# Performance work log

Hardware: AMD Instinct MI355X
Metric: run time of the kernel (lower is better)

The kernel has to match this reference:

```python
import jax, jax.numpy as jnp
import numpy as np

NUM_PRIMARY_CAPS = 8
PRIMARY_DIM = 8
NUM_CLASSES = 10
OUT_DIM = 16
CHANNELS = 32
NUM_ROUTING = 3
IN_UNITS1 = CHANNELS * 20 * 20  # 12800


def squash(s):
    # squash as written in the source: |s| / (1 + |s|^2) * s
    n = jnp.linalg.norm(s, axis=-1, keepdims=True)
    return n / (1.0 + n * n) * s


def routing(u_hat, num_routing):
    # u_hat: [B, num_caps, in_units, dim_caps]
    b = jnp.zeros(u_hat.shape[:3] + (1,), dtype=u_hat.dtype)
    v = None
    for it in range(num_routing):
        c = jax.nn.softmax(b, axis=1)                       # over num_caps
        s = jnp.sum(c * u_hat, axis=2, keepdims=True)        # [B,J,1,M]
        v = squash(s)
        if it < num_routing - 1:
            b = b + jnp.sum(u_hat * v, axis=-1, keepdims=True)
    return v[:, :, 0, :]                                     # [B, num_caps, dim_caps]


def setup_inputs() -> dict:
    key = jax.random.key(0)
    k1, k2, k3, k4, k5 = jax.random.split(key, 5)
    x = jax.random.normal(k1, (64, 1, 28, 28), dtype=jnp.float32)
    conv_w = jax.random.normal(k2, (CHANNELS, 1, 9, 9), dtype=jnp.float32) * 0.05
    conv_b = jax.random.normal(k3, (CHANNELS,), dtype=jnp.float32) * 0.05
    # W: [num_capsules, in_units, dim_capsules, in_channels]
    W1 = jax.random.normal(k4, (NUM_PRIMARY_CAPS, IN_UNITS1, PRIMARY_DIM, CHANNELS), dtype=jnp.float32) * 0.05
    W2 = jax.random.normal(k5, (NUM_CLASSES, NUM_PRIMARY_CAPS, OUT_DIM, PRIMARY_DIM), dtype=jnp.float32) * 0.05
    return {"x": x, "conv_w": conv_w, "conv_b": conv_b, "W1": W1, "W2": W2}


def reference(x, conv_w, conv_b, W1, W2):
    B = x.shape[0]
    # conv1 + relu: [B,1,28,28] -> [B,C,20,20]
    h = jax.lax.conv_general_dilated(
        x, conv_w, window_strides=(1, 1), padding='VALID',
        dimension_numbers=('NCHW', 'OIHW', 'NCHW'))
    h = jax.nn.relu(h + conv_b[None, :, None, None])
    # primary capsules: flatten features to in_units; the source einsum
    # 'ijkl,ijkm->ijkm' reduces W over its in_channels axis and broadcasts x,
    # so u_hat[b,j,k,m] = sum_c W1[j,k,m,c] * x[b,k]
    xf = h.reshape(B, IN_UNITS1)
    u1 = jnp.einsum('jkmc,bk->bjkm', W1, xf)   # [B, 8, 12800, primary_dim]
    v1 = routing(u1, 1)                         # [B, 8, primary_dim]
    # digit capsules: per-unit feature vectors, standard capsule transform
    u2 = jnp.einsum('jkmc,bkc->bjkm', W2, v1)   # [B, 10, 8, out_dim]
    v2 = routing(u2, NUM_ROUTING)               # [B, 10, out_dim]
    return v2
```

## Files before the change

kernel.cpp:

```cpp
#include <hip/hip_runtime.h>

typedef float f4 __attribute__((ext_vector_type(4)));

__device__ __forceinline__ float readlane_f(float v, int l) {
    return __int_as_float(__builtin_amdgcn_readlane(__float_as_int(v), l));
}

__device__ __forceinline__ void barrier_lds() {
    asm volatile("s_waitcnt lgkmcnt(0)\n\ts_barrier" ::: "memory");
}

__global__ __launch_bounds__(512) void fused_kernel(
    const float* __restrict__ X, const float* __restrict__ CW, const float* __restrict__ CB,
    const float* __restrict__ W1, float* __restrict__ S1P)
{
    int i = blockIdx.x;
    int c = i >> 3, p0 = (i & 7) * 50;
    int t = threadIdx.x;
    int wave = t >> 6, lane = t & 63;

    __shared__ float xs[64][309];
    __shared__ float xt[50][64];

    int py0 = p0 / 20;

    int k0 = c * 400 + p0;
    const f4* Wp = reinterpret_cast<const f4*>(W1) + (size_t)wave * 819200
                   + (size_t)k0 * 64 + lane;
    f4 pre[10];
    #pragma unroll
    for (int q = 0; q < 10; ++q)
        pre[q] = __builtin_nontemporal_load(Wp + (size_t)q * 64);

    float bias = CB[c];
    const float* wcg = CW + c * 81;
    float w[81];
    #pragma unroll
    for (int q = 0; q < 81; ++q) w[q] = wcg[q];

    {
        int b = t >> 3, q = t & 7;
        const f4* src = reinterpret_cast<const f4*>(X + (size_t)b * 784 + py0 * 28);
        #pragma unroll
        for (int s = 0; s < 10; ++s) {
            int idx4 = q + 8 * s;
            if (idx4 < 77) {
                f4 v = src[idx4];
                float* d = &xs[b][idx4 * 4];
                d[0] = v.x; d[1] = v.y; d[2] = v.z; d[3] = v.w;
            }
        }
    }
    barrier_lds();

    {
        int psub = wave, b = lane;
        for (int pl = psub; pl < 50; pl += 8) {
            int p = p0 + pl;
            int py = p / 20, px = p - py * 20;
            const float* xrow = &xs[b][(py - py0) * 28 + px];
            float acc = bias;
            #pragma unroll
            for (int dy = 0; dy < 9; ++dy)
                #pragma unroll
                for (int dx = 0; dx < 9; ++dx)
                    acc = fmaf(xrow[dy * 28 + dx], w[dy * 9 + dx], acc);
            xt[pl][b] = acc > 0.f ? acc : 0.f;
        }
    }
    barrier_lds();

    float acc[8] = {0.f,0.f,0.f,0.f,0.f,0.f,0.f,0.f};
    #pragma unroll
    for (int kk = 0; kk < 10; ++kk) {
        f4 wv = pre[kk];
        float xv = xt[kk][lane];
        float s = (wv.x + wv.y) + (wv.z + wv.w);
        s += __shfl_xor(s, 1);
        s += __shfl_xor(s, 2);
        s += __shfl_xor(s, 4);
        #pragma unroll
        for (int m = 0; m < 8; ++m)
            acc[m] = fmaf(xv, readlane_f(s, m * 8), acc[m]);
    }
    Wp += (size_t)10 * 64;
    #pragma unroll 10
    for (int kk = 10; kk < 50; ++kk) {
        f4 wv = __builtin_nontemporal_load(Wp); Wp += 64;
        float xv = xt[kk][lane];
        float s = (wv.x + wv.y) + (wv.z + wv.w);
        s += __shfl_xor(s, 1);
        s += __shfl_xor(s, 2);
        s += __shfl_xor(s, 4);
        #pragma unroll
        for (int m = 0; m < 8; ++m)
            acc[m] = fmaf(xv, readlane_f(s, m * 8), acc[m]);
    }

    float* dst = S1P + (((size_t)i * 64 + lane) * 8 + wave) * 8;
    f4 lo = {acc[0], acc[1], acc[2], acc[3]};
    f4 hi = {acc[4], acc[5], acc[6], acc[7]};
    reinterpret_cast<f4*>(dst)[0] = lo;
    reinterpret_cast<f4*>(dst)[1] = hi;
}

__global__ __launch_bounds__(256) void routing_kernel(
    const float* __restrict__ W2, const float* __restrict__ S1P,
    float* __restrict__ OUT)
{
    int b = blockIdx.x;
    int t = threadIdx.x;
    __shared__ float part[16][64];
    __shared__ float v1[64];
    __shared__ float u2[10][8][16];
    __shared__ float blog[10][8];
    __shared__ float cw[10][8];
    __shared__ float sv[10][16];
    __shared__ float vv[10][16];
    __shared__ float fac[16];

    {
        int q = t & 15, r = t >> 4;
        const f4* base = reinterpret_cast<const f4*>(S1P) + ((size_t)r * 64 + b) * 16 + q;
        f4 a = {0.f, 0.f, 0.f, 0.f};
        #pragma unroll
        for (int s = 0; s < 16; ++s)
            a += base[(size_t)s * 16384];
        part[r][q * 4 + 0] = a.x;
        part[r][q * 4 + 1] = a.y;
        part[r][q * 4 + 2] = a.z;
        part[r][q * 4 + 3] = a.w;
    }
    __syncthreads();
    if (t < 64) {
        float v = 0.f;
        #pragma unroll
        for (int r = 0; r < 16; ++r) v += part[r][t];
        v1[t] = v * 0.125f;
    }
    if (t >= 64 && t < 144) { int q = t - 64; blog[q >> 3][q & 7] = 0.f; }
    __syncthreads();
    if (t < 8) {
        float n2 = 0.f;
        #pragma unroll
        for (int m = 0; m < 8; ++m) { float x = v1[t * 8 + m]; n2 = fmaf(x, x, n2); }
        float n = sqrtf(n2);
        fac[t] = n / (1.f + n2);
    }
    __syncthreads();
    if (t < 64) v1[t] *= fac[t >> 3];
    __syncthreads();

    for (int idx = t; idx < 1280; idx += 256) {
        int j = idx >> 7;
        int r = idx & 127;
        int k = r >> 4, m = r & 15;
        const float* wp = W2 + idx * 8;
        float a = 0.f;
        #pragma unroll
        for (int cc = 0; cc < 8; ++cc) a = fmaf(wp[cc], v1[k * 8 + cc], a);
        u2[j][k][m] = a;
    }
    __syncthreads();

    for (int it = 0; it < 3; ++it) {
        if (t < 8) {
            float mx = -1e30f;
            #pragma unroll
            for (int j = 0; j < 10; ++j) mx = fmaxf(mx, blog[j][t]);
            float e[10], se = 0.f;
            #pragma unroll
            for (int j = 0; j < 10; ++j) { e[j] = expf(blog[j][t] - mx); se += e[j]; }
            float inv = 1.f / se;
            #pragma unroll
            for (int j = 0; j < 10; ++j) cw[j][t] = e[j] * inv;
        }
        __syncthreads();
        if (t < 160) {
            int j = t >> 4, m = t & 15;
            float a = 0.f;
            #pragma unroll
            for (int k = 0; k < 8; ++k) a = fmaf(cw[j][k], u2[j][k][m], a);
            sv[j][m] = a;
        }
        __syncthreads();
        if (t < 10) {
            float n2 = 0.f;
            #pragma unroll
            for (int m = 0; m < 16; ++m) { float x = sv[t][m]; n2 = fmaf(x, x, n2); }
            float n = sqrtf(n2);
            fac[t] = n / (1.f + n2);
        }
        __syncthreads();
        if (t < 160) { int j = t >> 4, m = t & 15; vv[j][m] = sv[j][m] * fac[j]; }
        __syncthreads();
        if (it < 2) {
            if (t < 80) {
                int j = t >> 3, k = t & 7;
                float d = 0.f;
                #pragma unroll
                for (int m = 0; m < 16; ++m) d = fmaf(u2[j][k][m], vv[j][m], d);
                blog[j][k] += d;
            }
            __syncthreads();
        }
    }
    if (t < 160) OUT[b * 160 + t] = vv[t >> 4][t & 15];
}

extern "C" void kernel_launch(void* const* d_in, const int* in_sizes, int n_in,
                              void* d_out, int out_size, void* d_ws, size_t ws_size,
                              hipStream_t stream) {
    const float* X  = (const float*)d_in[0];
    const float* CW = (const float*)d_in[1];
    const float* CB = (const float*)d_in[2];
    const float* W1 = (const float*)d_in[3];
    const float* W2 = (const float*)d_in[4];
    float* S1P = (float*)d_ws;
    float* OUT = (float*)d_out;

    fused_kernel<<<256, 512, 0, stream>>>(X, CW, CB, W1, S1P);
    routing_kernel<<<64, 256, 0, stream>>>(W2, S1P, OUT);
}
```

Baseline: 165.5 us.

## Fuse conv/primary-capsule and routing kernels via atomic grid-wide flag barrier

Merges the two launches into one kernel. Every block writes its partial sums and then increments a global counter. The first 64 blocks spin until all 256 blocks have arrived, then run the routing stage in the same launch. To make room for the routing shared memory, the conv input staging is halved to 32 batches and processed in two passes, and the partial-sum reduction is respread over 512 threads. This aims to remove the second launch and the gap between kernels, but it adds a memset launch and relies on all 256 blocks being co-resident to avoid deadlock.

```diff
diff --git a/kernel.cpp b/kernel.cpp
--- a/kernel.cpp
+++ b/kernel.cpp
@@ -10,17 +10,26 @@
     asm volatile("s_waitcnt lgkmcnt(0)\n\ts_barrier" ::: "memory");
 }
 
-__global__ __launch_bounds__(512) void fused_kernel(
+__global__ __launch_bounds__(512) void mega_kernel(
     const float* __restrict__ X, const float* __restrict__ CW, const float* __restrict__ CB,
-    const float* __restrict__ W1, float* __restrict__ S1P)
+    const float* __restrict__ W1, const float* __restrict__ W2,
+    float* __restrict__ S1P, unsigned int* __restrict__ FLAG, float* __restrict__ OUT)
 {
     int i = blockIdx.x;
     int c = i >> 3, p0 = (i & 7) * 50;
     int t = threadIdx.x;
     int wave = t >> 6, lane = t & 63;
 
-    __shared__ float xs[64][309];
+    __shared__ float xs[32][309];
     __shared__ float xt[50][64];
+    __shared__ float part[32][64];
+    __shared__ float v1[64];
+    __shared__ float u2[10][8][16];
+    __shared__ float blog[10][8];
+    __shared__ float cw[10][8];
+    __shared__ float sv[10][16];
+    __shared__ float vv[10][16];
+    __shared__ float fac[16];
 
     int py0 = p0 / 20;
 
@@ -38,37 +47,38 @@
     #pragma unroll
     for (int q = 0; q < 81; ++q) w[q] = wcg[q];
 
-    {
-        int b = t >> 3, q = t & 7;
-        const f4* src = reinterpret_cast<const f4*>(X + (size_t)b * 784 + py0 * 28);
-        #pragma unroll
-        for (int s = 0; s < 10; ++s) {
-            int idx4 = q + 8 * s;
-            if (idx4 < 77) {
-                f4 v = src[idx4];
-                float* d = &xs[b][idx4 * 4];
-                d[0] = v.x; d[1] = v.y; d[2] = v.z; d[3] = v.w;
+    for (int h = 0; h < 2; ++h) {
+        {
+            int b2 = t >> 4, q = t & 15;
+            const f4* src = reinterpret_cast<const f4*>(X + (size_t)(b2 + 32 * h) * 784 + py0 * 28);
+            #pragma unroll
+            for (int s = 0; s < 5; ++s) {
+                int idx4 = q + 16 * s;
+                if (idx4 < 77) {
+                    f4 v = src[idx4];
+                    float* d = &xs[b2][idx4 * 4];
+                    d[0] = v.x; d[1] = v.y; d[2] = v.z; d[3] = v.w;
+                }
             }
         }
-    }
-    barrier_lds();
-
-    {
-        int psub = wave, b = lane;
-        for (int pl = psub; pl < 50; pl += 8) {
-            int p = p0 + pl;
-            int py = p / 20, px = p - py * 20;
-            const float* xrow = &xs[b][(py - py0) * 28 + px];
-            float acc = bias;
-            #pragma unroll
-            for (int dy = 0; dy < 9; ++dy)
+        barrier_lds();
+        {
+            int psub = t >> 5, b2 = t & 31;
+            for (int pl = psub; pl < 50; pl += 16) {
+                int p = p0 + pl;
+                int py = p / 20, px = p - py * 20;
+                const float* xrow = &xs[b2][(py - py0) * 28 + px];
+                float acc = bias;
                 #pragma unroll
-                for (int dx = 0; dx < 9; ++dx)
-                    acc = fmaf(xrow[dy * 28 + dx], w[dy * 9 + dx], acc);
-            xt[pl][b] = acc > 0.f ? acc : 0.f;
-        }
-    }
-    barrier_lds();
+                for (int dy = 0; dy < 9; ++dy)
+                    #pragma unroll
+                    for (int dx = 0; dx < 9; ++dx)
+                        acc = fmaf(xrow[dy * 28 + dx], w[dy * 9 + dx], acc);
+                xt[pl][b2 + 32 * h] = acc > 0.f ? acc : 0.f;
+            }
+        }
+        barrier_lds();
+    }
 
     float acc[8] = {0.f,0.f,0.f,0.f,0.f,0.f,0.f,0.f};
     #pragma unroll
@@ -97,35 +107,36 @@
             acc[m] = fmaf(xv, readlane_f(s, m * 8), acc[m]);
     }
 
-    float* dst = S1P + (((size_t)i * 64 + lane) * 8 + wave) * 8;
-    f4 lo = {acc[0], acc[1], acc[2], acc[3]};
-    f4 hi = {acc[4], acc[5], acc[6], acc[7]};
-    reinterpret_cast<f4*>(dst)[0] = lo;
-    reinterpret_cast<f4*>(dst)[1] = hi;
-}
-
-__global__ __launch_bounds__(256) void routing_kernel(
-    const float* __restrict__ W2, const float* __restrict__ S1P,
-    float* __restrict__ OUT)
-{
-    int b = blockIdx.x;
-    int t = threadIdx.x;
-    __shared__ float part[16][64];
-    __shared__ float v1[64];
-    __shared__ float u2[10][8][16];
-    __shared__ float blog[10][8];
-    __shared__ float cw[10][8];
-    __shared__ float sv[10][16];
-    __shared__ float vv[10][16];
-    __shared__ float fac[16];
+    {
+        float* dst = S1P + (((size_t)i * 64 + lane) * 8 + wave) * 8;
+        f4 lo = {acc[0], acc[1], acc[2], acc[3]};
+        f4 hi = {acc[4], acc[5], acc[6], acc[7]};
+        reinterpret_cast<f4*>(dst)[0] = lo;
+        reinterpret_cast<f4*>(dst)[1] = hi;
+    }
+
+    __syncthreads();
+    if (t == 0) {
+        __threadfence();
+        atomicAdd(FLAG, 1u);
+    }
+    if (i >= 64) return;
+
+    int b = i;
+    if (t == 0) {
+        while (__hip_atomic_load(FLAG, __ATOMIC_ACQUIRE, __HIP_MEMORY_SCOPE_AGENT) < 256u)
+            __builtin_amdgcn_s_sleep(1);
+    }
+    __syncthreads();
+    __threadfence();
 
     {
         int q = t & 15, r = t >> 4;
         const f4* base = reinterpret_cast<const f4*>(S1P) + ((size_t)r * 64 + b) * 16 + q;
         f4 a = {0.f, 0.f, 0.f, 0.f};
         #pragma unroll
-        for (int s = 0; s < 16; ++s)
-            a += base[(size_t)s * 16384];
+        for (int s = 0; s < 8; ++s)
+            a += base[(size_t)s * 32768];
         part[r][q * 4 + 0] = a.x;
         part[r][q * 4 + 1] = a.y;
         part[r][q * 4 + 2] = a.z;
@@ -135,7 +146,7 @@
     if (t < 64) {
         float v = 0.f;
         #pragma unroll
-        for (int r = 0; r < 16; ++r) v += part[r][t];
+        for (int r = 0; r < 32; ++r) v += part[r][t];
         v1[t] = v * 0.125f;
     }
     if (t >= 64 && t < 144) { int q = t - 64; blog[q >> 3][q & 7] = 0.f; }
@@ -151,7 +162,7 @@
     if (t < 64) v1[t] *= fac[t >> 3];
     __syncthreads();
 
-    for (int idx = t; idx < 1280; idx += 256) {
+    for (int idx = t; idx < 1280; idx += 512) {
         int j = idx >> 7;
         int r = idx & 127;
         int k = r >> 4, m = r & 15;
@@ -217,8 +228,9 @@
     const float* W1 = (const float*)d_in[3];
     const float* W2 = (const float*)d_in[4];
     float* S1P = (float*)d_ws;
+    unsigned int* FLAG = (unsigned int*)((char*)d_ws + 4194304);
     float* OUT = (float*)d_out;
 
-    fused_kernel<<<256, 512, 0, stream>>>(X, CW, CB, W1, S1P);
-    routing_kernel<<<64, 256, 0, stream>>>(W2, S1P, OUT);
-}
+    hipMemsetAsync(FLAG, 0, 4, stream);
+    mega_kernel<<<256, 512, 0, stream>>>(X, CW, CB, W1, W2, S1P, FLAG, OUT);
+}
```

After: 194.3 us. 1.17x slower.
